# Kernel optimization log

Hardware: AMD Instinct MI355X
Metric: run time of the kernel (lower is better)

The kernel has to match this reference:

```python
import jax, jax.numpy as jnp
import numpy as np

N_NODES = 50000
N_EDGES = 400000
IN_CH = 165
HID = 64
HEADS = 8
EPS = 1e-5
NEG_SLOPE = 0.2


def _layer_norm(x, g, b):
    mu = jnp.mean(x, axis=-1, keepdims=True)
    var = jnp.mean(jnp.square(x - mu), axis=-1, keepdims=True)
    return (x - mu) * jax.lax.rsqrt(var + EPS) * g + b


def _gat_conv(x, src, dst, W, a_src, a_dst, bias, concat):
    # x: [N, F_in]; src/dst: [E] (self-loops already appended)
    N = x.shape[0]
    H, C = a_src.shape
    h = (x @ W).reshape(N, H, C)                       # [N, H, C]
    alpha_s = jnp.sum(h * a_src, axis=-1)              # [N, H]
    alpha_d = jnp.sum(h * a_dst, axis=-1)              # [N, H]
    e = jax.nn.leaky_relu(alpha_s[src] + alpha_d[dst], NEG_SLOPE)  # [E, H]
    # segment softmax over incoming edges of each dst node
    m = jax.ops.segment_max(e, dst, num_segments=N)    # [N, H]
    m = jnp.where(jnp.isfinite(m), m, 0.0)
    ex = jnp.exp(e - m[dst])                           # [E, H]
    denom = jax.ops.segment_sum(ex, dst, num_segments=N)  # [N, H]
    alpha = ex / denom[dst]                            # [E, H]
    out = jax.ops.segment_sum(alpha[:, :, None] * h[src], dst, num_segments=N)  # [N, H, C]
    if concat:
        out = out.reshape(N, H * C)
    else:
        out = out.mean(axis=1)
    return out + bias


def setup_inputs() -> dict:
    key = jax.random.key(0)
    ks = jax.random.split(key, 24)
    sc = 0.05
    d = {
        'x': jax.random.normal(ks[0], (N_NODES, IN_CH), dtype=jnp.float32),
        'edge_index': jax.random.randint(ks[1], (2, N_EDGES), 0, N_NODES, dtype=jnp.int64),
        # layer 0: in=165 -> heads*hid=512 (concat)
        'W0': jax.random.normal(ks[2], (IN_CH, HEADS * HID), jnp.float32) * sc,
        'as0': jax.random.normal(ks[3], (HEADS, HID), jnp.float32) * sc,
        'ad0': jax.random.normal(ks[4], (HEADS, HID), jnp.float32) * sc,
        'b0': jnp.zeros((HEADS * HID,), jnp.float32),
        'lng0': jnp.ones((HEADS * HID,), jnp.float32),
        'lnb0': jnp.zeros((HEADS * HID,), jnp.float32),
        # layer 1: 512 -> 512 (concat, residual applies)
        'W1': jax.random.normal(ks[5], (HEADS * HID, HEADS * HID), jnp.float32) * sc,
        'as1': jax.random.normal(ks[6], (HEADS, HID), jnp.float32) * sc,
        'ad1': jax.random.normal(ks[7], (HEADS, HID), jnp.float32) * sc,
        'b1': jnp.zeros((HEADS * HID,), jnp.float32),
        'lng1': jnp.ones((HEADS * HID,), jnp.float32),
        'lnb1': jnp.zeros((HEADS * HID,), jnp.float32),
        # layer 2: 512 -> 64 (mean over heads)
        'W2': jax.random.normal(ks[8], (HEADS * HID, HEADS * HID), jnp.float32) * sc,
        'as2': jax.random.normal(ks[9], (HEADS, HID), jnp.float32) * sc,
        'ad2': jax.random.normal(ks[10], (HEADS, HID), jnp.float32) * sc,
        'b2': jnp.zeros((HID,), jnp.float32),
        'lng2': jnp.ones((HID,), jnp.float32),
        'lnb2': jnp.zeros((HID,), jnp.float32),
        'lin_w': jax.random.normal(ks[11], (HID, 2), jnp.float32) * sc,
        'lin_b': jnp.zeros((2,), jnp.float32),
    }
    return d


def reference(x, edge_index, W0, as0, ad0, b0, lng0, lnb0,
              W1, as1, ad1, b1, lng1, lnb1,
              W2, as2, ad2, b2, lng2, lnb2, lin_w, lin_b):
    N = x.shape[0]
    loops = jnp.arange(N, dtype=edge_index.dtype)
    src = jnp.concatenate([edge_index[0], loops])
    dst = jnp.concatenate([edge_index[1], loops])

    layers = [
        (W0, as0, ad0, b0, lng0, lnb0, True),
        (W1, as1, ad1, b1, lng1, lnb1, True),
        (W2, as2, ad2, b2, lng2, lnb2, False),
    ]
    h = x
    for (W, a_s, a_d, b, g, bb, concat) in layers:
        residual = h
        h = _gat_conv(h, src, dst, W, a_s, a_d, b, concat)
        if h.shape == residual.shape:
            h = h + residual
        h = _layer_norm(h, g, bb)
        h = jax.nn.relu(h)
        # dropout is identity in eval mode
    return h @ lin_w + lin_b
```

## Files before the change

### kernel.cpp

```cpp
#include <hip/hip_runtime.h>
#include <hip/hip_bf16.h>
#include <cstdint>
#include <cstddef>

#define HEADS 8
#define HID 64
#define HF 512
#define NEG_SLOPE 0.2f
#define LN_EPS 1e-5f

typedef __hip_bfloat16 bf16;
typedef __attribute__((ext_vector_type(8))) __bf16 bf16v8;
typedef __attribute__((ext_vector_type(4))) float f32x4;

__device__ __forceinline__ float wsum64(float v) {
#pragma unroll
  for (int o = 32; o > 0; o >>= 1) v += __shfl_xor(v, o, 64);
  return v;
}
__device__ __forceinline__ int wsum64i(int v) {
#pragma unroll
  for (int o = 32; o > 0; o >>= 1) v += __shfl_xor(v, o, 64);
  return v;
}
__device__ __forceinline__ float leaky(float v) { return v >= 0.f ? v : NEG_SLOPE * v; }
__device__ __forceinline__ float bits2f(unsigned short u) {
  return __uint_as_float(((unsigned)u) << 16);
}
__device__ __forceinline__ unsigned short f2bits(float x) {
  union { bf16 h; unsigned short u; } bu;
  bu.h = __float2bfloat16(x);
  return bu.u;
}

__global__ __launch_bounds__(256)
void convert_count(const int* __restrict__ ei, int* __restrict__ esrc,
                   int* __restrict__ edst, int* __restrict__ counts, int E) {
  int e = blockIdx.x * 256 + threadIdx.x;
  if (e >= E) return;
  bool i64 = (ei[1] == 0) && (ei[3] == 0) && (ei[5] == 0) && (ei[7] == 0);
  int s, d;
  if (i64) { s = ei[2 * (size_t)e]; d = ei[2 * ((size_t)E + e)]; }
  else     { s = ei[e];             d = ei[E + e]; }
  esrc[e] = s; edst[e] = d;
  atomicAdd(&counts[d], 1);
}

#define SCAN_T 256
#define SCAN_EPT 4
#define SCAN_CHUNK (SCAN_T * SCAN_EPT)

__global__ __launch_bounds__(SCAN_T)
void scan_pass1(const int* __restrict__ counts, int* __restrict__ bsum, int N) {
  int b = blockIdx.x, t = threadIdx.x;
  int base = b * SCAN_CHUNK + t * SCAN_EPT;
  int s = 0;
#pragma unroll
  for (int i = 0; i < SCAN_EPT; ++i) {
    int idx = base + i;
    if (idx < N) s += counts[idx] + 1;
  }
  int lane = t & 63, w = t >> 6;
  int tot = wsum64i(s);
  __shared__ int ws[4];
  if (lane == 0) ws[w] = tot;
  __syncthreads();
  if (t == 0) bsum[b] = ws[0] + ws[1] + ws[2] + ws[3];
}

__global__ __launch_bounds__(64)
void scan_pass2(const int* __restrict__ bsum, int* __restrict__ boff, int NB) {
  int t = threadIdx.x;
  int own = t < NB ? bsum[t] : 0;
  int v = own;
#pragma unroll
  for (int o = 1; o < 64; o <<= 1) {
    int u = __shfl_up(v, o, 64);
    if (t >= o) v += u;
  }
  if (t < NB) boff[t] = v - own;
}

__global__ __launch_bounds__(SCAN_T)
void scan_pass3(const int* __restrict__ counts, const int* __restrict__ boff,
                int* __restrict__ row_ptr, int* __restrict__ cursor, int N, int Etot) {
  int b = blockIdx.x, t = threadIdx.x;
  int base = b * SCAN_CHUNK + t * SCAN_EPT;
  int c[SCAN_EPT];
  int s = 0;
#pragma unroll
  for (int i = 0; i < SCAN_EPT; ++i) {
    int idx = base + i;
    c[i] = idx < N ? counts[idx] + 1 : 0;
    s += c[i];
  }
  int lane = t & 63, w = t >> 6;
  int inc = s;
#pragma unroll
  for (int o = 1; o < 64; o <<= 1) {
    int u = __shfl_up(inc, o, 64);
    if (lane >= o) inc += u;
  }
  __shared__ int wsums[4];
  if (lane == 63) wsums[w] = inc;
  __syncthreads();
  int woff = 0;
  for (int i = 0; i < w; ++i) woff += wsums[i];
  int run = inc - s + woff + boff[b];
#pragma unroll
  for (int i = 0; i < SCAN_EPT; ++i) {
    int idx = base + i;
    if (idx < N) { row_ptr[idx] = run; cursor[idx] = run; run += c[i]; }
  }
  if (b == 0 && t == 0) row_ptr[N] = Etot;
}

__global__ __launch_bounds__(256)
void scatter_kernel(const int* __restrict__ esrc, const int* __restrict__ edst,
                    int* __restrict__ cursor, int* __restrict__ col, int N, int E) {
  int e = blockIdx.x * 256 + threadIdx.x;
  int Etot = E + N;
  if (e >= Etot) return;
  int s = e < E ? esrc[e] : e - E;
  int d = e < E ? edst[e] : e - E;
  int pos = atomicAdd(&cursor[d], 1);
  col[pos] = s;
}

__global__ __launch_bounds__(256)
void convert_pad_x(const float* __restrict__ x, bf16* __restrict__ xbf,
                   int M, int K, int Kp) {
  int idx = blockIdx.x * 256 + threadIdx.x;
  if (idx >= M * Kp) return;
  int row = idx / Kp, colk = idx - row * Kp;
  float v = colk < K ? x[(size_t)row * K + colk] : 0.f;
  xbf[idx] = __float2bfloat16(v);
}

__global__ __launch_bounds__(256)
void transpose_w(const float* __restrict__ W, bf16* __restrict__ Wt,
                 int K, int Ncols, int Kp) {
  int idx = blockIdx.x * 256 + threadIdx.x;
  if (idx >= Ncols * Kp) return;
  int n = idx / Kp, k = idx - n * Kp;
  float v = k < K ? W[(size_t)k * Ncols + n] : 0.f;
  Wt[idx] = __float2bfloat16(v);
}

#define LDSW 40
__global__ __launch_bounds__(256)
void gemm_mfma(const bf16* __restrict__ A, const bf16* __restrict__ Bt,
               bf16* __restrict__ C, int M, int Ncols, int K) {
  __shared__ short Alds[128 * LDSW];
  __shared__ short Blds[128 * LDSW];
  const int tid = threadIdx.x;
  const int wave = tid >> 6, lane = tid & 63;
  const int wr = wave >> 1, wc = wave & 1;
  const int row0 = blockIdx.x * 128, col0 = blockIdx.y * 128;
  const int lrow = lane & 15;
  const int kc = lane >> 4;
  f32x4 acc[4][4] = {};

  for (int k0 = 0; k0 < K; k0 += 32) {
#pragma unroll
    for (int i = 0; i < 2; ++i) {
      int idx = tid + i * 256;
      int r = idx >> 2, c4 = idx & 3;
      uint4 va = make_uint4(0, 0, 0, 0);
      int gm = row0 + r;
      if (gm < M) va = *reinterpret_cast<const uint4*>(A + (size_t)gm * K + k0 + c4 * 8);
      *reinterpret_cast<uint4*>(&Alds[r * LDSW + c4 * 8]) = va;
      uint4 vb = *reinterpret_cast<const uint4*>(Bt + (size_t)(col0 + r) * K + k0 + c4 * 8);
      *reinterpret_cast<uint4*>(&Blds[r * LDSW + c4 * 8]) = vb;
    }
    __syncthreads();
    bf16v8 af[4], bfr[4];
#pragma unroll
    for (int r = 0; r < 4; ++r)
      af[r] = *reinterpret_cast<const bf16v8*>(&Alds[(wr * 64 + r * 16 + lrow) * LDSW + kc * 8]);
#pragma unroll
    for (int c = 0; c < 4; ++c)
      bfr[c] = *reinterpret_cast<const bf16v8*>(&Blds[(wc * 64 + c * 16 + lrow) * LDSW + kc * 8]);
#pragma unroll
    for (int r = 0; r < 4; ++r)
#pragma unroll
      for (int c = 0; c < 4; ++c)
        acc[r][c] = __builtin_amdgcn_mfma_f32_16x16x32_bf16(af[r], bfr[c], acc[r][c], 0, 0, 0);
    __syncthreads();
  }

  const int crow = (lane >> 4) * 4;
  const int ccol = lane & 15;
#pragma unroll
  for (int r = 0; r < 4; ++r) {
#pragma unroll
    for (int c = 0; c < 4; ++c) {
      int gc = col0 + wc * 64 + c * 16 + ccol;
#pragma unroll
      for (int j = 0; j < 4; ++j) {
        int gr = row0 + wr * 64 + r * 16 + crow + j;
        if (gr < M) C[(size_t)gr * Ncols + gc] = __float2bfloat16(acc[r][c][j]);
      }
    }
  }
}

__global__ __launch_bounds__(256)
void alpha_kernel(const bf16* __restrict__ hbuf, const float* __restrict__ as,
                  const float* __restrict__ ad, float* __restrict__ alpha_s,
                  float* __restrict__ alpha_d, int N) {
  int wid = (blockIdx.x * 256 + threadIdx.x) >> 6;
  int lane = threadIdx.x & 63;
  if (wid >= N) return;
  ushort4 u0 = *reinterpret_cast<const ushort4*>(hbuf + (size_t)wid * HF + lane * 8);
  ushort4 u1 = *reinterpret_cast<const ushort4*>(hbuf + (size_t)wid * HF + lane * 8 + 4);
  float4 s0 = ((const float4*)as)[lane * 2], s1 = ((const float4*)as)[lane * 2 + 1];
  float4 d0 = ((const float4*)ad)[lane * 2], d1 = ((const float4*)ad)[lane * 2 + 1];
  float f0 = bits2f(u0.x), f1 = bits2f(u0.y), f2 = bits2f(u0.z), f3 = bits2f(u0.w);
  float f4 = bits2f(u1.x), f5 = bits2f(u1.y), f6 = bits2f(u1.z), f7 = bits2f(u1.w);
  float s = f0 * s0.x + f1 * s0.y + f2 * s0.z + f3 * s0.w
          + f4 * s1.x + f5 * s1.y + f6 * s1.z + f7 * s1.w;
  float d = f0 * d0.x + f1 * d0.y + f2 * d0.z + f3 * d0.w
          + f4 * d1.x + f5 * d1.y + f6 * d1.z + f7 * d1.w;
#pragma unroll
  for (int o = 1; o < 8; o <<= 1) {
    s += __shfl_xor(s, o, 64);
    d += __shfl_xor(d, o, 64);
  }
  if ((lane & 7) == 0) {
    alpha_s[wid * HEADS + (lane >> 3)] = s;
    alpha_d[wid * HEADS + (lane >> 3)] = d;
  }
}

template <int LAYER>
__global__ __launch_bounds__(128)
void aggregate_kernel(const int* __restrict__ row_ptr, const int* __restrict__ col,
                      const bf16* __restrict__ hbuf,
                      const float* __restrict__ alpha_s, const float* __restrict__ alpha_d,
                      const bf16* __restrict__ resid,
                      const float* __restrict__ bias, const float* __restrict__ g,
                      const float* __restrict__ b,
                      bf16* __restrict__ out_bf, int N) {
  int n = blockIdx.x;
  int t = threadIdx.x;
  int h = t >> 4;
  float adh = alpha_d[n * HEADS + h];
  float m = -1e30f, den = 0.f;
  float a0 = 0.f, a1 = 0.f, a2 = 0.f, a3 = 0.f;
  int lo = row_ptr[n], hi = row_ptr[n + 1];

  int sj = col[lo];
  float asj = alpha_s[sj * HEADS + h];
  ushort4 u = *reinterpret_cast<const ushort4*>(hbuf + (size_t)sj * HF + t * 4);

  for (int j = lo; j < hi; ++j) {
    float e = leaky(asj + adh);
    ushort4 uc = u;
    if (j + 1 < hi) {
      int sn = col[j + 1];
      asj = alpha_s[sn * HEADS + h];
      u = *reinterpret_cast<const ushort4*>(hbuf + (size_t)sn * HF + t * 4);
    }
    if (e > m) {
      float sc = __expf(m - e);
      den *= sc; a0 *= sc; a1 *= sc; a2 *= sc; a3 *= sc;
      m = e;
    }
    float ex = __expf(e - m);
    den += ex;
    a0 = fmaf(ex, bits2f(uc.x), a0);
    a1 = fmaf(ex, bits2f(uc.y), a1);
    a2 = fmaf(ex, bits2f(uc.z), a2);
    a3 = fmaf(ex, bits2f(uc.w), a3);
  }
  float inv = 1.f / den;
  a0 *= inv; a1 *= inv; a2 *= inv; a3 *= inv;

  if (LAYER < 2) {
    float4 bb = ((const float4*)bias)[t];
    a0 += bb.x; a1 += bb.y; a2 += bb.z; a3 += bb.w;
    if (LAYER == 1) {
      ushort4 r = *reinterpret_cast<const ushort4*>(resid + (size_t)n * HF + t * 4);
      a0 += bits2f(r.x); a1 += bits2f(r.y); a2 += bits2f(r.z); a3 += bits2f(r.w);
    }
    float s = a0 + a1 + a2 + a3;
    float ss = a0 * a0 + a1 * a1 + a2 * a2 + a3 * a3;
    s = wsum64(s); ss = wsum64(ss);
    __shared__ float sh[4];
    if ((t & 63) == 0) { sh[t >> 6] = s; sh[2 + (t >> 6)] = ss; }
    __syncthreads();
    float tot = sh[0] + sh[1], tot2 = sh[2] + sh[3];
    float mu = tot * (1.f / HF);
    float var = tot2 * (1.f / HF) - mu * mu;
    float rs = rsqrtf(var + LN_EPS);
    float4 gg = ((const float4*)g)[t];
    float4 be = ((const float4*)b)[t];
    a0 = fmaxf((a0 - mu) * rs * gg.x + be.x, 0.f);
    a1 = fmaxf((a1 - mu) * rs * gg.y + be.y, 0.f);
    a2 = fmaxf((a2 - mu) * rs * gg.z + be.z, 0.f);
    a3 = fmaxf((a3 - mu) * rs * gg.w + be.w, 0.f);
    ushort4 o;
    o.x = f2bits(a0); o.y = f2bits(a1); o.z = f2bits(a2); o.w = f2bits(a3);
    *reinterpret_cast<ushort4*>(out_bf + (size_t)n * HF + t * 4) = o;
  } else {
    __shared__ float lds[HF];
    lds[t * 4 + 0] = a0; lds[t * 4 + 1] = a1;
    lds[t * 4 + 2] = a2; lds[t * 4 + 3] = a3;
    __syncthreads();
    if (t < HID) {
      float v = 0.f;
#pragma unroll
      for (int hh = 0; hh < HEADS; ++hh) v += lds[hh * HID + t];
      v = v * (1.f / HEADS) + bias[t];
      float s = wsum64(v);
      float ss = wsum64(v * v);
      float mu = s * (1.f / HID);
      float var = ss * (1.f / HID) - mu * mu;
      float rs = rsqrtf(var + LN_EPS);
      v = fmaxf((v - mu) * rs * g[t] + b[t], 0.f);
      out_bf[(size_t)n * HID + t] = __float2bfloat16(v);
    }
  }
}

__global__ __launch_bounds__(256)
void final_linear_kernel(const bf16* __restrict__ D, const float* __restrict__ w,
                         const float* __restrict__ bb, float* __restrict__ out, int N) {
  int wid = (blockIdx.x * 256 + threadIdx.x) >> 6;
  int lane = threadIdx.x & 63;
  if (wid >= N) return;
  float v = __bfloat162float(D[(size_t)wid * HID + lane]);
  float s0 = wsum64(v * w[lane * 2 + 0]);
  float s1 = wsum64(v * w[lane * 2 + 1]);
  if (lane == 0) {
    out[(size_t)wid * 2 + 0] = s0 + bb[0];
    out[(size_t)wid * 2 + 1] = s1 + bb[1];
  }
}

extern "C" void kernel_launch(void* const* d_in, const int* in_sizes, int n_in,
                              void* d_out, int out_size, void* d_ws, size_t ws_size,
                              hipStream_t stream) {
  const float* x  = (const float*)d_in[0];
  const int*   ei = (const int*)d_in[1];
  const int N = in_sizes[0] / 165;
  const int E = in_sizes[1] / 2;
  const int Etot = E + N;
  const int K0P = 192;

  const float* W[3]  = {(const float*)d_in[2],  (const float*)d_in[8],  (const float*)d_in[14]};
  const float* As[3] = {(const float*)d_in[3],  (const float*)d_in[9],  (const float*)d_in[15]};
  const float* Ad[3] = {(const float*)d_in[4],  (const float*)d_in[10], (const float*)d_in[16]};
  const float* Bi[3] = {(const float*)d_in[5],  (const float*)d_in[11], (const float*)d_in[17]};
  const float* Lg[3] = {(const float*)d_in[6],  (const float*)d_in[12], (const float*)d_in[18]};
  const float* Lb[3] = {(const float*)d_in[7],  (const float*)d_in[13], (const float*)d_in[19]};
  const float* lin_w = (const float*)d_in[20];
  const float* lin_b = (const float*)d_in[21];

  char* p = (char*)d_ws;
  auto alloc = [&](size_t bytes) {
    char* r = p;
    p += (bytes + 255) & ~(size_t)255;
    return r;
  };
  bf16* feat0   = (bf16*)alloc((size_t)N * HF * 2);
  bf16* hbuf    = (bf16*)alloc((size_t)N * HF * 2);
  bf16* bufD    = (bf16*)alloc((size_t)N * HID * 2);
  float* alpha_s = (float*)alloc((size_t)N * HEADS * 4);
  float* alpha_d = (float*)alloc((size_t)N * HEADS * 4);
  bf16* W0t = (bf16*)alloc((size_t)HF * K0P * 2);
  bf16* W1t = (bf16*)alloc((size_t)HF * HF * 2);
  bf16* W2t = (bf16*)alloc((size_t)HF * HF * 2);
  int* esrc    = (int*)alloc((size_t)E * 4);
  int* edst    = (int*)alloc((size_t)E * 4);
  int* counts  = (int*)alloc((size_t)N * 4);
  int* row_ptr = (int*)alloc((size_t)(N + 1) * 4);
  int* cursor  = (int*)alloc((size_t)N * 4);
  int* col     = (int*)alloc((size_t)Etot * 4);
  int* bsum    = (int*)alloc((size_t)256 * 4);
  int* boff    = (int*)alloc((size_t)256 * 4);
  (void)ws_size;

  bf16* xbf = feat0;

  const int NB = (N + SCAN_CHUNK - 1) / SCAN_CHUNK;

  hipMemsetAsync(counts, 0, (size_t)N * 4, stream);
  convert_count<<<(E + 255) / 256, 256, 0, stream>>>(ei, esrc, edst, counts, E);
  scan_pass1<<<NB, SCAN_T, 0, stream>>>(counts, bsum, N);
  scan_pass2<<<1, 64, 0, stream>>>(bsum, boff, NB);
  scan_pass3<<<NB, SCAN_T, 0, stream>>>(counts, boff, row_ptr, cursor, N, Etot);
  scatter_kernel<<<(Etot + 255) / 256, 256, 0, stream>>>(esrc, edst, cursor, col, N, E);

  convert_pad_x<<<((N * K0P) + 255) / 256, 256, 0, stream>>>(x, xbf, N, 165, K0P);
  transpose_w<<<((HF * K0P) + 255) / 256, 256, 0, stream>>>(W[0], W0t, 165, HF, K0P);
  transpose_w<<<((HF * HF) + 255) / 256, 256, 0, stream>>>(W[1], W1t, HF, HF, HF);
  transpose_w<<<((HF * HF) + 255) / 256, 256, 0, stream>>>(W[2], W2t, HF, HF, HF);

  dim3 ggrid((N + 127) / 128, HF / 128);
  const int waveBlocks = (N + 3) / 4;

  gemm_mfma<<<ggrid, 256, 0, stream>>>(xbf, W0t, hbuf, N, HF, K0P);
  alpha_kernel<<<waveBlocks, 256, 0, stream>>>(hbuf, As[0], Ad[0], alpha_s, alpha_d, N);
  aggregate_kernel<0><<<N, 128, 0, stream>>>(row_ptr, col, hbuf, alpha_s, alpha_d,
                                             nullptr, Bi[0], Lg[0], Lb[0], feat0, N);

  gemm_mfma<<<ggrid, 256, 0, stream>>>(feat0, W1t, hbuf, N, HF, HF);
  alpha_kernel<<<waveBlocks, 256, 0, stream>>>(hbuf, As[1], Ad[1], alpha_s, alpha_d, N);
  aggregate_kernel<1><<<N, 128, 0, stream>>>(row_ptr, col, hbuf, alpha_s, alpha_d,
                                             feat0, Bi[1], Lg[1], Lb[1], feat0, N);

  gemm_mfma<<<ggrid, 256, 0, stream>>>(feat0, W2t, hbuf, N, HF, HF);
  alpha_kernel<<<waveBlocks, 256, 0, stream>>>(hbuf, As[2], Ad[2], alpha_s, alpha_d, N);
  aggregate_kernel<2><<<N, 128, 0, stream>>>(row_ptr, col, hbuf, alpha_s, alpha_d,
                                             nullptr, Bi[2], Lg[2], Lb[2], bufD, N);

  final_linear_kernel<<<waveBlocks, 256, 0, stream>>>(bufD, lin_w, lin_b, (float*)d_out, N);
}
```

Measured before the change: 512.8 us.

## Fuse attention-logit dots into GEMM epilogue; aggregate one node per wave

The per-head attention dot products alpha_s/alpha_d are now computed in the GEMM epilogue from the fp32 accumulators using cross-lane shuffles. This removes the separate alpha_kernel and its full re-read of hbuf in every layer. The aggregation kernel now maps one node to a 64-lane wave, with 4 nodes per 256-thread block and 8 bf16 per lane via 16-byte loads. This drops the block-level LDS reduction and __syncthreads for layer norm, at the cost of more registers per lane and slightly different rounding, since alpha is now taken from fp32 values rather than the bf16-stored ones.

```diff
diff --git a/kernel.cpp b/kernel.cpp
--- a/kernel.cpp
+++ b/kernel.cpp
@@ -150,7 +150,10 @@
 #define LDSW 40
 __global__ __launch_bounds__(256)
 void gemm_mfma(const bf16* __restrict__ A, const bf16* __restrict__ Bt,
-               bf16* __restrict__ C, int M, int Ncols, int K) {
+               bf16* __restrict__ C,
+               const float* __restrict__ as_g, const float* __restrict__ ad_g,
+               float* __restrict__ alpha_s, float* __restrict__ alpha_d,
+               int M, int Ncols, int K) {
   __shared__ short Alds[128 * LDSW];
   __shared__ short Blds[128 * LDSW];
   const int tid = threadIdx.x;
@@ -203,38 +206,42 @@
       }
     }
   }
-}
-
-__global__ __launch_bounds__(256)
-void alpha_kernel(const bf16* __restrict__ hbuf, const float* __restrict__ as,
-                  const float* __restrict__ ad, float* __restrict__ alpha_s,
-                  float* __restrict__ alpha_d, int N) {
-  int wid = (blockIdx.x * 256 + threadIdx.x) >> 6;
-  int lane = threadIdx.x & 63;
-  if (wid >= N) return;
-  ushort4 u0 = *reinterpret_cast<const ushort4*>(hbuf + (size_t)wid * HF + lane * 8);
-  ushort4 u1 = *reinterpret_cast<const ushort4*>(hbuf + (size_t)wid * HF + lane * 8 + 4);
-  float4 s0 = ((const float4*)as)[lane * 2], s1 = ((const float4*)as)[lane * 2 + 1];
-  float4 d0 = ((const float4*)ad)[lane * 2], d1 = ((const float4*)ad)[lane * 2 + 1];
-  float f0 = bits2f(u0.x), f1 = bits2f(u0.y), f2 = bits2f(u0.z), f3 = bits2f(u0.w);
-  float f4 = bits2f(u1.x), f5 = bits2f(u1.y), f6 = bits2f(u1.z), f7 = bits2f(u1.w);
-  float s = f0 * s0.x + f1 * s0.y + f2 * s0.z + f3 * s0.w
-          + f4 * s1.x + f5 * s1.y + f6 * s1.z + f7 * s1.w;
-  float d = f0 * d0.x + f1 * d0.y + f2 * d0.z + f3 * d0.w
-          + f4 * d1.x + f5 * d1.y + f6 * d1.z + f7 * d1.w;
-#pragma unroll
-  for (int o = 1; o < 8; o <<= 1) {
-    s += __shfl_xor(s, o, 64);
-    d += __shfl_xor(d, o, 64);
-  }
-  if ((lane & 7) == 0) {
-    alpha_s[wid * HEADS + (lane >> 3)] = s;
-    alpha_d[wid * HEADS + (lane >> 3)] = d;
+
+  const int head = (col0 + wc * 64) >> 6;
+  float asf[4], adf[4];
+#pragma unroll
+  for (int c = 0; c < 4; ++c) {
+    asf[c] = as_g[head * HID + c * 16 + ccol];
+    adf[c] = ad_g[head * HID + c * 16 + ccol];
+  }
+#pragma unroll
+  for (int r = 0; r < 4; ++r) {
+#pragma unroll
+    for (int j = 0; j < 4; ++j) {
+      float ps = 0.f, pd = 0.f;
+#pragma unroll
+      for (int c = 0; c < 4; ++c) {
+        ps = fmaf(acc[r][c][j], asf[c], ps);
+        pd = fmaf(acc[r][c][j], adf[c], pd);
+      }
+#pragma unroll
+      for (int o = 1; o < 16; o <<= 1) {
+        ps += __shfl_xor(ps, o, 64);
+        pd += __shfl_xor(pd, o, 64);
+      }
+      if (ccol == 0) {
+        int gr = row0 + wr * 64 + r * 16 + crow + j;
+        if (gr < M) {
+          alpha_s[gr * HEADS + head] = ps;
+          alpha_d[gr * HEADS + head] = pd;
+        }
+      }
+    }
   }
 }
 
 template <int LAYER>
-__global__ __launch_bounds__(128)
+__global__ __launch_bounds__(256)
 void aggregate_kernel(const int* __restrict__ row_ptr, const int* __restrict__ col,
                       const bf16* __restrict__ hbuf,
                       const float* __restrict__ alpha_s, const float* __restrict__ alpha_d,
@@ -242,85 +249,90 @@
                       const float* __restrict__ bias, const float* __restrict__ g,
                       const float* __restrict__ b,
                       bf16* __restrict__ out_bf, int N) {
-  int n = blockIdx.x;
-  int t = threadIdx.x;
-  int h = t >> 4;
+  int w = threadIdx.x >> 6;
+  int lane = threadIdx.x & 63;
+  int nn = blockIdx.x * 4 + w;
+  bool valid = nn < N;
+  int n = valid ? nn : 0;
+  int h = lane >> 3;
   float adh = alpha_d[n * HEADS + h];
   float m = -1e30f, den = 0.f;
-  float a0 = 0.f, a1 = 0.f, a2 = 0.f, a3 = 0.f;
+  float a[8] = {};
   int lo = row_ptr[n], hi = row_ptr[n + 1];
 
   int sj = col[lo];
   float asj = alpha_s[sj * HEADS + h];
-  ushort4 u = *reinterpret_cast<const ushort4*>(hbuf + (size_t)sj * HF + t * 4);
+  uint4 u = *reinterpret_cast<const uint4*>(hbuf + (size_t)sj * HF + lane * 8);
 
   for (int j = lo; j < hi; ++j) {
     float e = leaky(asj + adh);
-    ushort4 uc = u;
+    uint4 uc = u;
     if (j + 1 < hi) {
       int sn = col[j + 1];
       asj = alpha_s[sn * HEADS + h];
-      u = *reinterpret_cast<const ushort4*>(hbuf + (size_t)sn * HF + t * 4);
+      u = *reinterpret_cast<const uint4*>(hbuf + (size_t)sn * HF + lane * 8);
     }
     if (e > m) {
       float sc = __expf(m - e);
-      den *= sc; a0 *= sc; a1 *= sc; a2 *= sc; a3 *= sc;
+      den *= sc;
+#pragma unroll
+      for (int i = 0; i < 8; ++i) a[i] *= sc;
       m = e;
     }
     float ex = __expf(e - m);
     den += ex;
-    a0 = fmaf(ex, bits2f(uc.x), a0);
-    a1 = fmaf(ex, bits2f(uc.y), a1);
-    a2 = fmaf(ex, bits2f(uc.z), a2);
-    a3 = fmaf(ex, bits2f(uc.w), a3);
+    const unsigned short* us = reinterpret_cast<const unsigned short*>(&uc);
+#pragma unroll
+    for (int i = 0; i < 8; ++i) a[i] = fmaf(ex, bits2f(us[i]), a[i]);
   }
   float inv = 1.f / den;
-  a0 *= inv; a1 *= inv; a2 *= inv; a3 *= inv;
+#pragma unroll
+  for (int i = 0; i < 8; ++i) a[i] *= inv;
 
   if (LAYER < 2) {
-    float4 bb = ((const float4*)bias)[t];
-    a0 += bb.x; a1 += bb.y; a2 += bb.z; a3 += bb.w;
+    float4 b0 = ((const float4*)bias)[lane * 2];
+    float4 b1 = ((const float4*)bias)[lane * 2 + 1];
+    a[0] += b0.x; a[1] += b0.y; a[2] += b0.z; a[3] += b0.w;
+    a[4] += b1.x; a[5] += b1.y; a[6] += b1.z; a[7] += b1.w;
     if (LAYER == 1) {
-      ushort4 r = *reinterpret_cast<const ushort4*>(resid + (size_t)n * HF + t * 4);
-      a0 += bits2f(r.x); a1 += bits2f(r.y); a2 += bits2f(r.z); a3 += bits2f(r.w);
-    }
-    float s = a0 + a1 + a2 + a3;
-    float ss = a0 * a0 + a1 * a1 + a2 * a2 + a3 * a3;
+      uint4 rr = *reinterpret_cast<const uint4*>(resid + (size_t)n * HF + lane * 8);
+      const unsigned short* rs = reinterpret_cast<const unsigned short*>(&rr);
+#pragma unroll
+      for (int i = 0; i < 8; ++i) a[i] += bits2f(rs[i]);
+    }
+    float s = 0.f, ss = 0.f;
+#pragma unroll
+    for (int i = 0; i < 8; ++i) { s += a[i]; ss += a[i] * a[i]; }
     s = wsum64(s); ss = wsum64(ss);
-    __shared__ float sh[4];
-    if ((t & 63) == 0) { sh[t >> 6] = s; sh[2 + (t >> 6)] = ss; }
-    __syncthreads();
-    float tot = sh[0] + sh[1], tot2 = sh[2] + sh[3];
-    float mu = tot * (1.f / HF);
-    float var = tot2 * (1.f / HF) - mu * mu;
+    float mu = s * (1.f / HF);
+    float var = ss * (1.f / HF) - mu * mu;
     float rs = rsqrtf(var + LN_EPS);
-    float4 gg = ((const float4*)g)[t];
-    float4 be = ((const float4*)b)[t];
-    a0 = fmaxf((a0 - mu) * rs * gg.x + be.x, 0.f);
-    a1 = fmaxf((a1 - mu) * rs * gg.y + be.y, 0.f);
-    a2 = fmaxf((a2 - mu) * rs * gg.z + be.z, 0.f);
-    a3 = fmaxf((a3 - mu) * rs * gg.w + be.w, 0.f);
-    ushort4 o;
-    o.x = f2bits(a0); o.y = f2bits(a1); o.z = f2bits(a2); o.w = f2bits(a3);
-    *reinterpret_cast<ushort4*>(out_bf + (size_t)n * HF + t * 4) = o;
+    float4 g0 = ((const float4*)g)[lane * 2], g1 = ((const float4*)g)[lane * 2 + 1];
+    float4 e0 = ((const float4*)b)[lane * 2], e1 = ((const float4*)b)[lane * 2 + 1];
+    float gg[8] = {g0.x, g0.y, g0.z, g0.w, g1.x, g1.y, g1.z, g1.w};
+    float be[8] = {e0.x, e0.y, e0.z, e0.w, e1.x, e1.y, e1.z, e1.w};
+    unsigned short o[8];
+#pragma unroll
+    for (int i = 0; i < 8; ++i)
+      o[i] = f2bits(fmaxf((a[i] - mu) * rs * gg[i] + be[i], 0.f));
+    if (valid)
+      *reinterpret_cast<uint4*>(out_bf + (size_t)n * HF + lane * 8) =
+          *reinterpret_cast<const uint4*>(o);
   } else {
-    __shared__ float lds[HF];
-    lds[t * 4 + 0] = a0; lds[t * 4 + 1] = a1;
-    lds[t * 4 + 2] = a2; lds[t * 4 + 3] = a3;
-    __syncthreads();
-    if (t < HID) {
-      float v = 0.f;
-#pragma unroll
-      for (int hh = 0; hh < HEADS; ++hh) v += lds[hh * HID + t];
-      v = v * (1.f / HEADS) + bias[t];
-      float s = wsum64(v);
-      float ss = wsum64(v * v);
-      float mu = s * (1.f / HID);
-      float var = ss * (1.f / HID) - mu * mu;
-      float rs = rsqrtf(var + LN_EPS);
-      v = fmaxf((v - mu) * rs * g[t] + b[t], 0.f);
-      out_bf[(size_t)n * HID + t] = __float2bfloat16(v);
-    }
+    __shared__ float lds[4][HF];
+#pragma unroll
+    for (int i = 0; i < 8; ++i) lds[w][lane * 8 + i] = a[i];
+    float v = 0.f;
+#pragma unroll
+    for (int hh = 0; hh < HEADS; ++hh) v += lds[w][hh * HID + lane];
+    v = v * (1.f / HEADS) + bias[lane];
+    float s = wsum64(v);
+    float ss = wsum64(v * v);
+    float mu = s * (1.f / HID);
+    float var = ss * (1.f / HID) - mu * mu;
+    float rs = rsqrtf(var + LN_EPS);
+    v = fmaxf((v - mu) * rs * g[lane] + b[lane], 0.f);
+    if (valid) out_bf[(size_t)n * HID + lane] = __float2bfloat16(v);
   }
 }
 
@@ -399,22 +411,23 @@
   transpose_w<<<((HF * HF) + 255) / 256, 256, 0, stream>>>(W[2], W2t, HF, HF, HF);
 
   dim3 ggrid((N + 127) / 128, HF / 128);
+  const int aggBlocks  = (N + 3) / 4;
   const int waveBlocks = (N + 3) / 4;
 
-  gemm_mfma<<<ggrid, 256, 0, stream>>>(xbf, W0t, hbuf, N, HF, K0P);
-  alpha_kernel<<<waveBlocks, 256, 0, stream>>>(hbuf, As[0], Ad[0], alpha_s, alpha_d, N);
-  aggregate_kernel<0><<<N, 128, 0, stream>>>(row_ptr, col, hbuf, alpha_s, alpha_d,
-                                             nullptr, Bi[0], Lg[0], Lb[0], feat0, N);
-
-  gemm_mfma<<<ggrid, 256, 0, stream>>>(feat0, W1t, hbuf, N, HF, HF);
-  alpha_kernel<<<waveBlocks, 256, 0, stream>>>(hbuf, As[1], Ad[1], alpha_s, alpha_d, N);
-  aggregate_kernel<1><<<N, 128, 0, stream>>>(row_ptr, col, hbuf, alpha_s, alpha_d,
-                                             feat0, Bi[1], Lg[1], Lb[1], feat0, N);
-
-  gemm_mfma<<<ggrid, 256, 0, stream>>>(feat0, W2t, hbuf, N, HF, HF);
-  alpha_kernel<<<waveBlocks, 256, 0, stream>>>(hbuf, As[2], Ad[2], alpha_s, alpha_d, N);
-  aggregate_kernel<2><<<N, 128, 0, stream>>>(row_ptr, col, hbuf, alpha_s, alpha_d,
-                                             nullptr, Bi[2], Lg[2], Lb[2], bufD, N);
+  gemm_mfma<<<ggrid, 256, 0, stream>>>(xbf, W0t, hbuf, As[0], Ad[0],
+                                       alpha_s, alpha_d, N, HF, K0P);
+  aggregate_kernel<0><<<aggBlocks, 256, 0, stream>>>(row_ptr, col, hbuf, alpha_s, alpha_d,
+                                                     nullptr, Bi[0], Lg[0], Lb[0], feat0, N);
+
+  gemm_mfma<<<ggrid, 256, 0, stream>>>(feat0, W1t, hbuf, As[1], Ad[1],
+                                       alpha_s, alpha_d, N, HF, HF);
+  aggregate_kernel<1><<<aggBlocks, 256, 0, stream>>>(row_ptr, col, hbuf, alpha_s, alpha_d,
+                                                     feat0, Bi[1], Lg[1], Lb[1], feat0, N);
+
+  gemm_mfma<<<ggrid, 256, 0, stream>>>(feat0, W2t, hbuf, As[2], Ad[2],
+                                       alpha_s, alpha_d, N, HF, HF);
+  aggregate_kernel<2><<<aggBlocks, 256, 0, stream>>>(row_ptr, col, hbuf, alpha_s, alpha_d,
+                                                     nullptr, Bi[2], Lg[2], Lb[2], bufD, N);
 
   final_linear_kernel<<<waveBlocks, 256, 0, stream>>>(bufD, lin_w, lin_b, (float*)d_out, N);
 }
```

Result: no change. 516.4 us (+0.7%).
